# Optimization experiments

Hardware: AMD Instinct MI355X
Metric: run time of the kernel (lower is better)

## Reference

```python
import jax, jax.numpy as jnp
import numpy as np

T = 20.0
SCALE = 0.3


def setup_inputs() -> dict:
    key = jax.random.key(0)
    ks = jax.random.split(key, 6)
    B, C = 16384, 1000
    inp = {f"outputs{i+1}": jax.random.normal(ks[i], (B, C), dtype=jnp.float32) for i in range(5)}
    inp["targets"] = jax.random.randint(ks[5], (B,), 0, C, dtype=jnp.int64)
    return inp


def reference(outputs1, outputs2, outputs3, outputs4, outputs5, targets):
    # [5, B, C] stacked softmax predictions at temperature T
    preds = jnp.stack([outputs1, outputs2, outputs3, outputs4, outputs5], axis=0)
    preds = jax.nn.softmax(preds / T, axis=-1)
    # center over class dim and L2-normalize -> Pearson correlation via dot product
    v = preds - jnp.mean(preds, axis=-1, keepdims=True)            # [M,B,C]
    v = v / jnp.sqrt(jnp.sum(v * v, axis=-1, keepdims=True))       # [M,B,C]
    corr = jnp.einsum("mbc,nbc->mnb", v, v)                        # [M,M,B]
    M = preds.shape[0]
    iu, ju = jnp.triu_indices(M, k=1)
    d = jnp.sum(corr[iu, ju, :], axis=0)                            # [B] sum over pairs
    return jnp.mean(SCALE * d)
```

## Files before the change

### kernel.cpp

```cpp
#include <hip/hip_runtime.h>


#define CDIM   1000
#define C4DIM  250
#define NMODEL 5
#define T_INV  (1.0f / 20.0f)
#define INV_C  (1.0f / 1000.0f)
#define SCALEF 0.3f

__device__ __forceinline__ float wave_sum_f32(float v) {
    #pragma unroll
    for (int off = 32; off >= 1; off >>= 1)
        v += __shfl_xor(v, off);
    return v;
}

__global__ __launch_bounds__(256) void diversity_rows(
    const float* __restrict__ o1, const float* __restrict__ o2,
    const float* __restrict__ o3, const float* __restrict__ o4,
    const float* __restrict__ o5, float* __restrict__ ws, int B)
{
    const int lane = threadIdx.x & 63;
    const int wid  = threadIdx.x >> 6;
    const int b    = blockIdx.x * 4 + wid;
    if (b >= B) return;

    const bool act3 = lane < (C4DIM - 192);

    const size_t roff = (size_t)b * CDIM;
    const float4* r4[NMODEL] = {
        reinterpret_cast<const float4*>(o1 + roff),
        reinterpret_cast<const float4*>(o2 + roff),
        reinterpret_cast<const float4*>(o3 + roff),
        reinterpret_cast<const float4*>(o4 + roff),
        reinterpret_cast<const float4*>(o5 + roff)};

    float e[NMODEL][16];
    #pragma unroll
    for (int m = 0; m < NMODEL; ++m) {
        #pragma unroll
        for (int k = 0; k < 4; ++k) {
            float4 t = make_float4(0.0f, 0.0f, 0.0f, 0.0f);
            if (k < 3 || act3) t = r4[m][lane + 64 * k];
            e[m][4 * k + 0] = t.x; e[m][4 * k + 1] = t.y;
            e[m][4 * k + 2] = t.z; e[m][4 * k + 3] = t.w;
        }
    }

    float lsum[NMODEL];
    #pragma unroll
    for (int m = 0; m < NMODEL; ++m) {
        float a = 0.0f;
        #pragma unroll
        for (int i = 0; i < 16; ++i) {
            float ev = __expf(e[m][i] * T_INV);
            if (i >= 12 && !act3) ev = 0.0f;
            e[m][i] = ev;
            a += ev;
        }
        lsum[m] = a;
    }
    #pragma unroll
    for (int off = 32; off >= 1; off >>= 1) {
        #pragma unroll
        for (int m = 0; m < NMODEL; ++m)
            lsum[m] += __shfl_xor(lsum[m], off);
    }
    float rS[NMODEL];
    #pragma unroll
    for (int m = 0; m < NMODEL; ++m) rS[m] = 1.0f / lsum[m];

    float lss[NMODEL];
    #pragma unroll
    for (int m = 0; m < NMODEL; ++m) {
        float a = 0.0f;
        #pragma unroll
        for (int i = 0; i < 16; ++i) {
            float v = e[m][i] * rS[m] - INV_C;
            if (i >= 12 && !act3) v = 0.0f;
            e[m][i] = v;
            a += v * v;
        }
        lss[m] = a;
    }
    #pragma unroll
    for (int off = 32; off >= 1; off >>= 1) {
        #pragma unroll
        for (int m = 0; m < NMODEL; ++m)
            lss[m] += __shfl_xor(lss[m], off);
    }
    float rn[NMODEL];
    #pragma unroll
    for (int m = 0; m < NMODEL; ++m) rn[m] = 1.0f / sqrtf(lss[m]);

    float ssl = 0.0f;
    #pragma unroll
    for (int i = 0; i < 16; ++i) {
        float si = e[0][i] * rn[0];
        #pragma unroll
        for (int m = 1; m < NMODEL; ++m) si += e[m][i] * rn[m];
        ssl += si * si;
    }
    const float ss = wave_sum_f32(ssl);
    if (lane == 0)
        ws[b] = SCALEF * 0.5f * (ss - (float)NMODEL);
}

__global__ __launch_bounds__(1024) void final_reduce(
    const float* __restrict__ ws, float* __restrict__ out, int B)
{
    __shared__ double sm[1024];
    double acc = 0.0;
    for (int i = threadIdx.x; i < B; i += 1024)
        acc += (double)ws[i];
    sm[threadIdx.x] = acc;
    __syncthreads();
    #pragma unroll
    for (int s = 512; s > 0; s >>= 1) {
        if (threadIdx.x < s) sm[threadIdx.x] += sm[threadIdx.x + s];
        __syncthreads();
    }
    if (threadIdx.x == 0)
        out[0] = (float)(sm[0] / (double)B);
}

extern "C" void kernel_launch(void* const* d_in, const int* in_sizes, int n_in,
                              void* d_out, int out_size, void* d_ws, size_t ws_size,
                              hipStream_t stream)
{
    const float* o1 = (const float*)d_in[0];
    const float* o2 = (const float*)d_in[1];
    const float* o3 = (const float*)d_in[2];
    const float* o4 = (const float*)d_in[3];
    const float* o5 = (const float*)d_in[4];

    float* ws  = (float*)d_ws;
    float* out = (float*)d_out;

    const int B = in_sizes[0] / CDIM;

    diversity_rows<<<(B + 3) / 4, 256, 0, stream>>>(o1, o2, o3, o4, o5, ws, B);
    final_reduce<<<1, 1024, 0, stream>>>(ws, out, B);
}
```

Baseline: 65.22 us.

## Assign one row per 256-thread block with shared-memory cross-wave reductions

Each row is now processed by a full 256-thread block, with each thread loading one float4 per model, instead of one wavefront handling a row with four float4 loads per model. Per-thread register use drops and more loads are spread across threads, which should raise occupancy and memory-level parallelism. In exchange the kernel adds three __syncthreads and shared-memory reductions per row, launches four times as many blocks, and leaves 6 of 256 threads idle.

```diff
diff --git a/kernel.cpp b/kernel.cpp
--- a/kernel.cpp
+++ b/kernel.cpp
@@ -8,54 +8,48 @@
 #define INV_C  (1.0f / 1000.0f)
 #define SCALEF 0.3f
 
-__device__ __forceinline__ float wave_sum_f32(float v) {
-    #pragma unroll
-    for (int off = 32; off >= 1; off >>= 1)
-        v += __shfl_xor(v, off);
-    return v;
-}
-
 __global__ __launch_bounds__(256) void diversity_rows(
     const float* __restrict__ o1, const float* __restrict__ o2,
     const float* __restrict__ o3, const float* __restrict__ o4,
-    const float* __restrict__ o5, float* __restrict__ ws, int B)
+    const float* __restrict__ o5, float* __restrict__ ws)
 {
-    const int lane = threadIdx.x & 63;
-    const int wid  = threadIdx.x >> 6;
-    const int b    = blockIdx.x * 4 + wid;
-    if (b >= B) return;
+    const int b    = blockIdx.x;
+    const int t    = threadIdx.x;
+    const int wv   = t >> 6;
+    const int lane = t & 63;
+    const bool act = t < C4DIM;
+    const int idx  = act ? t : 0;
 
-    const bool act3 = lane < (C4DIM - 192);
+    __shared__ float redA[4][NMODEL];
+    __shared__ float redB[4][NMODEL];
+    __shared__ float redC[4];
 
     const size_t roff = (size_t)b * CDIM;
-    const float4* r4[NMODEL] = {
-        reinterpret_cast<const float4*>(o1 + roff),
-        reinterpret_cast<const float4*>(o2 + roff),
-        reinterpret_cast<const float4*>(o3 + roff),
-        reinterpret_cast<const float4*>(o4 + roff),
-        reinterpret_cast<const float4*>(o5 + roff)};
 
-    float e[NMODEL][16];
-    #pragma unroll
-    for (int m = 0; m < NMODEL; ++m) {
+    float e[NMODEL][4];
+    {
+        const float4* p[NMODEL] = {
+            reinterpret_cast<const float4*>(o1 + roff),
+            reinterpret_cast<const float4*>(o2 + roff),
+            reinterpret_cast<const float4*>(o3 + roff),
+            reinterpret_cast<const float4*>(o4 + roff),
+            reinterpret_cast<const float4*>(o5 + roff)};
         #pragma unroll
-        for (int k = 0; k < 4; ++k) {
-            float4 t = make_float4(0.0f, 0.0f, 0.0f, 0.0f);
-            if (k < 3 || act3) t = r4[m][lane + 64 * k];
-            e[m][4 * k + 0] = t.x; e[m][4 * k + 1] = t.y;
-            e[m][4 * k + 2] = t.z; e[m][4 * k + 3] = t.w;
+        for (int m = 0; m < NMODEL; ++m) {
+            float4 v = p[m][idx];
+            e[m][0] = v.x; e[m][1] = v.y; e[m][2] = v.z; e[m][3] = v.w;
         }
     }
+    __builtin_amdgcn_sched_barrier(0);
 
     float lsum[NMODEL];
     #pragma unroll
     for (int m = 0; m < NMODEL; ++m) {
         float a = 0.0f;
         #pragma unroll
-        for (int i = 0; i < 16; ++i) {
-            float ev = __expf(e[m][i] * T_INV);
-            if (i >= 12 && !act3) ev = 0.0f;
-            e[m][i] = ev;
+        for (int j = 0; j < 4; ++j) {
+            float ev = act ? __expf(e[m][j] * T_INV) : 0.0f;
+            e[m][j] = ev;
             a += ev;
         }
         lsum[m] = a;
@@ -66,19 +60,25 @@
         for (int m = 0; m < NMODEL; ++m)
             lsum[m] += __shfl_xor(lsum[m], off);
     }
+    if (lane == 0) {
+        #pragma unroll
+        for (int m = 0; m < NMODEL; ++m) redA[wv][m] = lsum[m];
+    }
+    __syncthreads();
+
     float rS[NMODEL];
     #pragma unroll
-    for (int m = 0; m < NMODEL; ++m) rS[m] = 1.0f / lsum[m];
+    for (int m = 0; m < NMODEL; ++m)
+        rS[m] = 1.0f / (redA[0][m] + redA[1][m] + redA[2][m] + redA[3][m]);
 
     float lss[NMODEL];
     #pragma unroll
     for (int m = 0; m < NMODEL; ++m) {
         float a = 0.0f;
         #pragma unroll
-        for (int i = 0; i < 16; ++i) {
-            float v = e[m][i] * rS[m] - INV_C;
-            if (i >= 12 && !act3) v = 0.0f;
-            e[m][i] = v;
+        for (int j = 0; j < 4; ++j) {
+            float v = act ? (e[m][j] * rS[m] - INV_C) : 0.0f;
+            e[m][j] = v;
             a += v * v;
         }
         lss[m] = a;
@@ -89,21 +89,35 @@
         for (int m = 0; m < NMODEL; ++m)
             lss[m] += __shfl_xor(lss[m], off);
     }
+    if (lane == 0) {
+        #pragma unroll
+        for (int m = 0; m < NMODEL; ++m) redB[wv][m] = lss[m];
+    }
+    __syncthreads();
+
     float rn[NMODEL];
     #pragma unroll
-    for (int m = 0; m < NMODEL; ++m) rn[m] = 1.0f / sqrtf(lss[m]);
+    for (int m = 0; m < NMODEL; ++m)
+        rn[m] = 1.0f / sqrtf(redB[0][m] + redB[1][m] + redB[2][m] + redB[3][m]);
 
     float ssl = 0.0f;
     #pragma unroll
-    for (int i = 0; i < 16; ++i) {
-        float si = e[0][i] * rn[0];
+    for (int j = 0; j < 4; ++j) {
+        float si = e[0][j] * rn[0];
         #pragma unroll
-        for (int m = 1; m < NMODEL; ++m) si += e[m][i] * rn[m];
+        for (int m = 1; m < NMODEL; ++m) si += e[m][j] * rn[m];
         ssl += si * si;
     }
-    const float ss = wave_sum_f32(ssl);
-    if (lane == 0)
+    #pragma unroll
+    for (int off = 32; off >= 1; off >>= 1)
+        ssl += __shfl_xor(ssl, off);
+    if (lane == 0) redC[wv] = ssl;
+    __syncthreads();
+
+    if (t == 0) {
+        float ss = redC[0] + redC[1] + redC[2] + redC[3];
         ws[b] = SCALEF * 0.5f * (ss - (float)NMODEL);
+    }
 }
 
 __global__ __launch_bounds__(1024) void final_reduce(
@@ -139,6 +153,6 @@
 
     const int B = in_sizes[0] / CDIM;
 
-    diversity_rows<<<(B + 3) / 4, 256, 0, stream>>>(o1, o2, o3, o4, o5, ws, B);
+    diversity_rows<<<B, 256, 0, stream>>>(o1, o2, o3, o4, o5, ws);
     final_reduce<<<1, 1024, 0, stream>>>(ws, out, B);
 }
```

Result: slower. 86.51 us (+32.7%).

## Compute per-row correlations from one-pass moment sums with double-buffered loads

Applied to the files above, without the earlier changes.

Replaces the three-pass softmax, center, normalize and dot pipeline with one streaming pass. The pass accumulates per-model sums and the pairwise products of shifted exponentials (exp(x/T)-1). Pearson correlations are then reconstructed in double precision from these moments after a single wave reduction. Loads are software-pipelined with a two-stage register buffer and a sched barrier, so fewer values stay live in registers. In exchange the shuffle reduction now carries 20 values instead of 5+5+1, and the moment formula risks cancellation, which the exp-1 shift and the double-precision finish are meant to limit.

```diff
diff --git a/kernel.cpp b/kernel.cpp
--- a/kernel.cpp
+++ b/kernel.cpp
@@ -3,17 +3,10 @@
 
 #define CDIM   1000
 #define C4DIM  250
-#define NMODEL 5
+#define NM     5
+#define NP     15
 #define T_INV  (1.0f / 20.0f)
-#define INV_C  (1.0f / 1000.0f)
 #define SCALEF 0.3f
-
-__device__ __forceinline__ float wave_sum_f32(float v) {
-    #pragma unroll
-    for (int off = 32; off >= 1; off >>= 1)
-        v += __shfl_xor(v, off);
-    return v;
-}
 
 __global__ __launch_bounds__(256) void diversity_rows(
     const float* __restrict__ o1, const float* __restrict__ o2,
@@ -26,84 +19,105 @@
     if (b >= B) return;
 
     const bool act3 = lane < (C4DIM - 192);
-
     const size_t roff = (size_t)b * CDIM;
-    const float4* r4[NMODEL] = {
+    const float4* base[NM] = {
         reinterpret_cast<const float4*>(o1 + roff),
         reinterpret_cast<const float4*>(o2 + roff),
         reinterpret_cast<const float4*>(o3 + roff),
         reinterpret_cast<const float4*>(o4 + roff),
         reinterpret_cast<const float4*>(o5 + roff)};
 
-    float e[NMODEL][16];
+    float A[NM];
+    float Bv[NP];
     #pragma unroll
-    for (int m = 0; m < NMODEL; ++m) {
+    for (int i = 0; i < NM; ++i) A[i] = 0.0f;
+    #pragma unroll
+    for (int p = 0; p < NP; ++p) Bv[p] = 0.0f;
+
+    float4 xb[2][NM];
+
+    #pragma unroll
+    for (int m = 0; m < NM; ++m)
+        xb[0][m] = base[m][lane];
+
+    #pragma unroll
+    for (int k = 0; k < 4; ++k) {
+        const int cur = k & 1;
+        const int nxt = cur ^ 1;
+
+        if (k + 1 < 4) {
+            if (k + 1 == 3) {
+                #pragma unroll
+                for (int m = 0; m < NM; ++m) {
+                    float4 t = make_float4(0.0f, 0.0f, 0.0f, 0.0f);
+                    if (act3) t = base[m][lane + 192];
+                    xb[nxt][m] = t;
+                }
+            } else {
+                #pragma unroll
+                for (int m = 0; m < NM; ++m)
+                    xb[nxt][m] = base[m][lane + 64 * (k + 1)];
+            }
+        }
+        __builtin_amdgcn_sched_barrier(0);
+
+        float u[NM][4];
         #pragma unroll
-        for (int k = 0; k < 4; ++k) {
-            float4 t = make_float4(0.0f, 0.0f, 0.0f, 0.0f);
-            if (k < 3 || act3) t = r4[m][lane + 64 * k];
-            e[m][4 * k + 0] = t.x; e[m][4 * k + 1] = t.y;
-            e[m][4 * k + 2] = t.z; e[m][4 * k + 3] = t.w;
+        for (int m = 0; m < NM; ++m) {
+            float4 v = xb[cur][m];
+            u[m][0] = __expf(v.x * T_INV) - 1.0f;
+            u[m][1] = __expf(v.y * T_INV) - 1.0f;
+            u[m][2] = __expf(v.z * T_INV) - 1.0f;
+            u[m][3] = __expf(v.w * T_INV) - 1.0f;
+        }
+        #pragma unroll
+        for (int c = 0; c < 4; ++c) {
+            #pragma unroll
+            for (int i = 0; i < NM; ++i) A[i] += u[i][c];
+            int p = 0;
+            #pragma unroll
+            for (int i = 0; i < NM; ++i) {
+                #pragma unroll
+                for (int j = i; j < NM; ++j) {
+                    Bv[p] = fmaf(u[i][c], u[j][c], Bv[p]);
+                    ++p;
+                }
+            }
         }
     }
 
-    float lsum[NMODEL];
-    #pragma unroll
-    for (int m = 0; m < NMODEL; ++m) {
-        float a = 0.0f;
-        #pragma unroll
-        for (int i = 0; i < 16; ++i) {
-            float ev = __expf(e[m][i] * T_INV);
-            if (i >= 12 && !act3) ev = 0.0f;
-            e[m][i] = ev;
-            a += ev;
-        }
-        lsum[m] = a;
-    }
     #pragma unroll
     for (int off = 32; off >= 1; off >>= 1) {
         #pragma unroll
-        for (int m = 0; m < NMODEL; ++m)
-            lsum[m] += __shfl_xor(lsum[m], off);
+        for (int i = 0; i < NM; ++i) A[i] += __shfl_xor(A[i], off);
+        #pragma unroll
+        for (int p = 0; p < NP; ++p) Bv[p] += __shfl_xor(Bv[p], off);
     }
-    float rS[NMODEL];
-    #pragma unroll
-    for (int m = 0; m < NMODEL; ++m) rS[m] = 1.0f / lsum[m];
 
-    float lss[NMODEL];
-    #pragma unroll
-    for (int m = 0; m < NMODEL; ++m) {
-        float a = 0.0f;
+    {
+        const double Cd = (double)CDIM;
+        double Ad[NM], den[NM];
         #pragma unroll
-        for (int i = 0; i < 16; ++i) {
-            float v = e[m][i] * rS[m] - INV_C;
-            if (i >= 12 && !act3) v = 0.0f;
-            e[m][i] = v;
-            a += v * v;
+        for (int i = 0; i < NM; ++i) Ad[i] = (double)A[i];
+        const int diag[NM] = {0, 5, 9, 12, 14};
+        #pragma unroll
+        for (int i = 0; i < NM; ++i)
+            den[i] = sqrt(Cd * (double)Bv[diag[i]] - Ad[i] * Ad[i]);
+
+        double d = 0.0;
+        int p = 0;
+        #pragma unroll
+        for (int i = 0; i < NM; ++i) {
+            #pragma unroll
+            for (int j = i; j < NM; ++j) {
+                if (j > i)
+                    d += (Cd * (double)Bv[p] - Ad[i] * Ad[j]) / (den[i] * den[j]);
+                ++p;
+            }
         }
-        lss[m] = a;
+        if (lane == 0)
+            ws[b] = (float)((double)SCALEF * d);
     }
-    #pragma unroll
-    for (int off = 32; off >= 1; off >>= 1) {
-        #pragma unroll
-        for (int m = 0; m < NMODEL; ++m)
-            lss[m] += __shfl_xor(lss[m], off);
-    }
-    float rn[NMODEL];
-    #pragma unroll
-    for (int m = 0; m < NMODEL; ++m) rn[m] = 1.0f / sqrtf(lss[m]);
-
-    float ssl = 0.0f;
-    #pragma unroll
-    for (int i = 0; i < 16; ++i) {
-        float si = e[0][i] * rn[0];
-        #pragma unroll
-        for (int m = 1; m < NMODEL; ++m) si += e[m][i] * rn[m];
-        ssl += si * si;
-    }
-    const float ss = wave_sum_f32(ssl);
-    if (lane == 0)
-        ws[b] = SCALEF * 0.5f * (ss - (float)NMODEL);
 }
 
 __global__ __launch_bounds__(1024) void final_reduce(
```

Result: slower. 72.02 us (+10.4%).
